# Optimization experiments

Hardware: AMD Instinct MI355X
Metric: run time of the kernel (lower is better)

The kernel has to match this reference:

```python
import jax, jax.numpy as jnp
import numpy as np

B, T, DM, DK = 16, 2048, 1024, 128

def setup_inputs() -> dict:
    key = jax.random.key(0)
    k1, k2, k3, k4 = jax.random.split(key, 4)
    x = jax.random.normal(k1, (B, T, DM), dtype=jnp.float32)
    # Linear(dm, dk, bias=False) weights, stored as [dm, dk] for x @ W
    scale = 1.0 / np.sqrt(DM)
    W_q = jax.random.normal(k2, (DM, DK), dtype=jnp.float32) * scale
    W_k = jax.random.normal(k3, (DM, DK), dtype=jnp.float32) * scale
    W_v = jax.random.normal(k4, (DM, DK), dtype=jnp.float32) * scale
    return {"x": x, "W_q": W_q, "W_k": W_k, "W_v": W_v}

def reference(x, W_q, W_k, W_v):
    # q, k, v: [B, T, DK]
    q = jnp.einsum('btd,dk->btk', x, W_q)
    k = jnp.einsum('btd,dk->btk', x, W_k)
    v = jnp.einsum('btd,dk->btk', x, W_v)
    dk = k.shape[-1]
    # scores: [B, T, T], scaled by dk**-0.5
    wei = jnp.einsum('bqk,bsk->bqs', q, k) * (dk ** -0.5)
    # causal mask (tril == 0 -> -inf)
    causal = jnp.tril(jnp.ones((q.shape[1], q.shape[1]), dtype=bool))
    wei = jnp.where(causal, wei, -jnp.inf)
    wei = jax.nn.softmax(wei, axis=-1)
    out = jnp.einsum('bqs,bsk->bqk', wei, v)  # [B, T, DK]
    return out
```

## Files before the change

kernel.cpp:

```cpp
#include <hip/hip_runtime.h>
#include <hip/hip_bf16.h>

#define NB 16
#define NT 2048
#define NDM 1024
#define NDK 128

typedef __bf16 bf16;
typedef bf16 bf16x4 __attribute__((ext_vector_type(4)));
typedef bf16 bf16x8 __attribute__((ext_vector_type(8)));
typedef float f32x4 __attribute__((ext_vector_type(4)));

__device__ inline bf16 to_bf16(float f) {
    __hip_bfloat16 h = __float2bfloat16(f);
    return *reinterpret_cast<bf16*>(&h);
}

__device__ inline void gload_lds16(const void* g, void* l) {
    __builtin_amdgcn_global_load_lds(
        (const __attribute__((address_space(1))) unsigned int*)g,
        (__attribute__((address_space(3))) unsigned int*)l, 16, 0, 0);
}

#define VMCNT(n) asm volatile("s_waitcnt vmcnt(" #n ")" ::: "memory")
#define LGKM0()  asm volatile("s_waitcnt lgkmcnt(0)" ::: "memory")
#define SCHEDB() __builtin_amdgcn_sched_barrier(0)

__global__ __launch_bounds__(256) void transpose_w_kernel(
        const float* __restrict__ Wq, const float* __restrict__ Wk,
        const float* __restrict__ Wv, bf16* __restrict__ Wt) {
    int idx = blockIdx.x * 256 + threadIdx.x;
    int w = idx >> 17;
    int r = idx & (NDM * NDK - 1);
    int k = r >> 7;
    int n = r & (NDK - 1);
    const float* W = (w == 0) ? Wq : ((w == 1) ? Wk : Wv);
    Wt[(size_t)w * NDK * NDM + (size_t)n * NDM + k] = to_bf16(W[(size_t)k * NDK + n]);
}

__global__ __launch_bounds__(512, 2) void proj_fused_kernel(
        const float* __restrict__ x, const bf16* __restrict__ Wt,
        bf16* __restrict__ qkv, bf16* __restrict__ Vt) {
    __shared__ __align__(16) char smem[65536];
    const int tid = threadIdx.x;
    const int lane = tid & 63, wave = tid >> 6;
    const int wr = wave >> 2, wc = wave & 3;
    const int r16 = lane & 15, kg = lane >> 4;
    const int mb = blockIdx.x;
    const float* xA = x + (size_t)mb * 128 * NDM;

    auto ASB = [&](int b) -> bf16* { return (bf16*)(smem + b * 8192); };
    auto BSB = [&](int b) -> bf16* { return (bf16*)(smem + 16384 + b * 24576); };

    const int a_row = tid >> 2, a_c = tid & 3;
    const int a_dst = (a_row * 4 + (a_c ^ ((a_row >> 1) & 3))) * 8;
    const size_t a_src = (size_t)a_row * NDM + a_c * 8;

    float4 alo, ahi;
    auto loadA = [&](int kt) {
        const float* src = xA + a_src + kt * 32;
        alo = *reinterpret_cast<const float4*>(src);
        ahi = *reinterpret_cast<const float4*>(src + 4);
    };
    auto writeA = [&](int buf) {
        bf16x8 v;
        v[0] = to_bf16(alo.x); v[1] = to_bf16(alo.y); v[2] = to_bf16(alo.z); v[3] = to_bf16(alo.w);
        v[4] = to_bf16(ahi.x); v[5] = to_bf16(ahi.y); v[6] = to_bf16(ahi.z); v[7] = to_bf16(ahi.w);
        *reinterpret_cast<bf16x8*>(ASB(buf) + a_dst) = v;
    };
    auto stageB = [&](int buf, int kt) {
#pragma unroll
        for (int p = 0; p < 3; p++) {
            int cid = p * 512 + tid;
            int w = cid >> 9, rem = cid & 511;
            int row = rem >> 2, c = rem & 3;
            int cs = c ^ ((row >> 1) & 3);
            gload_lds16(Wt + (size_t)w * NDK * NDM + (size_t)row * NDM + kt * 32 + cs * 8,
                        BSB(buf) + (size_t)(p * 512 + wave * 64) * 8);
        }
    };

    f32x4 acc[3][4][2];
#pragma unroll
    for (int w = 0; w < 3; w++)
#pragma unroll
        for (int m = 0; m < 4; m++)
#pragma unroll
            for (int n = 0; n < 2; n++) acc[w][m][n] = (f32x4){0.f, 0.f, 0.f, 0.f};

    loadA(0); SCHEDB(); stageB(0, 0); SCHEDB();
    VMCNT(3);
    writeA(0);
    loadA(1); SCHEDB(); stageB(1, 1); SCHEDB();
    VMCNT(5);
    LGKM0();
    __builtin_amdgcn_s_barrier();

    for (int kt = 0; kt < 32; kt++) {
        const int cur = kt & 1;
        bf16x8 af[4];
#pragma unroll
        for (int m = 0; m < 4; m++) {
            int arow = wr * 64 + m * 16 + r16;
            int ch = kg ^ ((arow >> 1) & 3);
            af[m] = *reinterpret_cast<const bf16x8*>(ASB(cur) + (arow * 4 + ch) * 8);
        }
#pragma unroll
        for (int w = 0; w < 3; w++) {
#pragma unroll
            for (int n = 0; n < 2; n++) {
                int brow = wc * 32 + n * 16 + r16;
                int ch = kg ^ ((brow >> 1) & 3);
                bf16x8 bfw = *reinterpret_cast<const bf16x8*>(
                    BSB(cur) + ((w * 128 + brow) * 4 + ch) * 8);
#pragma unroll
                for (int m = 0; m < 4; m++)
                    acc[w][m][n] = __builtin_amdgcn_mfma_f32_16x16x32_bf16(af[m], bfw, acc[w][m][n], 0, 0, 0);
            }
        }

        if (kt + 1 < 32) {
            VMCNT(3);
            writeA(1 - cur);
            LGKM0();
            __builtin_amdgcn_s_barrier();
            if (kt + 2 < 32) {
                loadA(kt + 2); SCHEDB(); stageB(cur, kt + 2); SCHEDB();
                VMCNT(5);
            } else {
                VMCNT(0);
            }
        }
    }

    __syncthreads();
    bf16 (*Tl)[136] = reinterpret_cast<bf16(*)[136]>(smem);
#pragma unroll
    for (int w = 0; w < 2; w++) {
        bf16* outw = qkv + (size_t)w * (size_t)(NB * NT) * NDK;
#pragma unroll
        for (int m = 0; m < 4; m++) {
            int rowb = mb * 128 + wr * 64 + m * 16 + kg * 4;
#pragma unroll
            for (int n = 0; n < 2; n++) {
                int col = wc * 32 + n * 16 + r16;
#pragma unroll
                for (int r = 0; r < 4; r++)
                    outw[(size_t)(rowb + r) * NDK + col] = to_bf16(acc[w][m][n][r]);
            }
        }
    }
#pragma unroll
    for (int m = 0; m < 4; m++) {
        int tl = wr * 64 + m * 16 + kg * 4;
#pragma unroll
        for (int n = 0; n < 2; n++) {
            int d = wc * 32 + n * 16 + r16;
            bf16x4 pv = { to_bf16(acc[2][m][n][0]), to_bf16(acc[2][m][n][1]),
                          to_bf16(acc[2][m][n][2]), to_bf16(acc[2][m][n][3]) };
            *reinterpret_cast<bf16x4*>(&Tl[d][tl]) = pv;
        }
    }
    __syncthreads();
    const int b = mb >> 4;
    const int t0 = (mb & 15) * 128;
    bf16* Vb = Vt + (size_t)b * NDK * NT;
#pragma unroll
    for (int p = 0; p < 4; p++) {
        int idx = p * 512 + tid;
        int d = idx >> 4, c = idx & 15;
        *reinterpret_cast<bf16x8*>(&Vb[(size_t)d * NT + t0 + c * 8]) =
            *reinterpret_cast<const bf16x8*>(&Tl[d][c * 8]);
    }
}

__global__ __launch_bounds__(256) void attn_kernel(
        const bf16* __restrict__ Q, const bf16* __restrict__ K,
        const bf16* __restrict__ Vt, float* __restrict__ out) {
    __shared__ bf16 Ks[2][64][128];
    __shared__ bf16 Vs[2][128][64];
    __shared__ bf16 Ps[4][16][72];
    const int tid = threadIdx.x, lane = tid & 63, wave = tid >> 6;
    const int r16 = lane & 15, kg = lane >> 4;

    const int bid = blockIdx.x;
    const int xcd = bid & 7;
    const int j = bid >> 3;
    const int b = xcd * 2 + (j & 1);
    const int qb = (NT / 64 - 1) - (j >> 1);
    const int q0 = qb * 64;
    const size_t baseB = (size_t)b * NT * NDK;
    const size_t baseVt = (size_t)b * NDK * NT;

    const float scale = 0.08838834764831843f;
    bf16x8 qf[4];
    const int qglob = q0 + wave * 16 + r16;
#pragma unroll
    for (int kc = 0; kc < 4; kc++) {
        bf16x8 raw = *reinterpret_cast<const bf16x8*>(&Q[baseB + (size_t)qglob * NDK + kc * 32 + kg * 8]);
#pragma unroll
        for (int jj = 0; jj < 8; jj++) raw[jj] = to_bf16((float)raw[jj] * scale);
        qf[kc] = raw;
    }

    f32x4 o[8];
#pragma unroll
    for (int n = 0; n < 8; n++) o[n] = (f32x4){0.f, 0.f, 0.f, 0.f};
    float mrun = -INFINITY;
    float lrun = 0.f;

    int krow[4], kcol[4], vrow[4], vcol[4];
#pragma unroll
    for (int i = 0; i < 4; i++) {
        int idx = i * 256 + tid;
        krow[i] = idx >> 4; kcol[i] = idx & 15;
        vrow[i] = idx >> 3; vcol[i] = idx & 7;
    }

    const int nsteps = qb + 1;
    bf16x8 kreg[4], vreg[4];
#pragma unroll
    for (int i = 0; i < 4; i++) {
        kreg[i] = *reinterpret_cast<const bf16x8*>(&K[baseB + (size_t)krow[i] * NDK + kcol[i] * 8]);
        vreg[i] = *reinterpret_cast<const bf16x8*>(&Vt[baseVt + (size_t)vrow[i] * NT + vcol[i] * 8]);
    }
#pragma unroll
    for (int i = 0; i < 4; i++) {
        *reinterpret_cast<bf16x8*>(&Ks[0][krow[i]][(kcol[i] ^ (krow[i] & 7)) * 8]) = kreg[i];
        *reinterpret_cast<bf16x8*>(&Vs[0][vrow[i]][(vcol[i] ^ (vrow[i] & 7)) * 8]) = vreg[i];
    }
    if (nsteps > 1) {
#pragma unroll
        for (int i = 0; i < 4; i++) {
            kreg[i] = *reinterpret_cast<const bf16x8*>(&K[baseB + (size_t)(64 + krow[i]) * NDK + kcol[i] * 8]);
            vreg[i] = *reinterpret_cast<const bf16x8*>(&Vt[baseVt + (size_t)vrow[i] * NT + 64 + vcol[i] * 8]);
        }
    }
    __syncthreads();

    for (int s = 0; s < nsteps; s++) {
        const int cur = s & 1;
        const int kv0 = s * 64;

        f32x4 sfr[4];
#pragma unroll
        for (int n = 0; n < 4; n++) sfr[n] = (f32x4){0.f, 0.f, 0.f, 0.f};
#pragma unroll
        for (int n = 0; n < 4; n++) {
            const int krw = n * 16 + r16;
#pragma unroll
            for (int kc = 0; kc < 4; kc++) {
                bf16x8 kf = *reinterpret_cast<const bf16x8*>(&Ks[cur][krw][((kc * 4 + kg) ^ (krw & 7)) * 8]);
                sfr[n] = __builtin_amdgcn_mfma_f32_16x16x32_bf16(kf, qf[kc], sfr[n], 0, 0, 0);
            }
        }

        if (s == nsteps - 1) {
#pragma unroll
            for (int n = 0; n < 4; n++)
#pragma unroll
                for (int r = 0; r < 4; r++)
                    if (kv0 + n * 16 + kg * 4 + r > qglob) sfr[n][r] = -INFINITY;
        }

        float pm = -INFINITY;
#pragma unroll
        for (int n = 0; n < 4; n++) {
            float t0 = fmaxf(fmaxf(sfr[n][0], sfr[n][1]), fmaxf(sfr[n][2], sfr[n][3]));
            pm = fmaxf(pm, t0);
        }
        pm = fmaxf(pm, __shfl_xor(pm, 16, 64));
        pm = fmaxf(pm, __shfl_xor(pm, 32, 64));

        if (__any(pm > mrun)) {
            float mnew = fmaxf(mrun, pm);
            float corr = __expf(mrun - mnew);
            mrun = mnew;
            lrun *= corr;
            float co[4];
#pragma unroll
            for (int r = 0; r < 4; r++) co[r] = __shfl(corr, kg * 4 + r, 64);
#pragma unroll
            for (int n = 0; n < 8; n++)
#pragma unroll
                for (int r = 0; r < 4; r++) o[n][r] *= co[r];
        }

        float ps = 0.f;
#pragma unroll
        for (int n = 0; n < 4; n++) {
            bf16x4 pw;
#pragma unroll
            for (int r = 0; r < 4; r++) {
                float pv = __expf(sfr[n][r] - mrun);
                ps += pv;
                pw[r] = to_bf16(pv);
            }
            *reinterpret_cast<bf16x4*>(&Ps[wave][r16][n * 16 + kg * 4]) = pw;
        }
        ps += __shfl_xor(ps, 16, 64);
        ps += __shfl_xor(ps, 32, 64);
        lrun += ps;

#pragma unroll
        for (int kc2 = 0; kc2 < 2; kc2++) {
            bf16x8 pf = *reinterpret_cast<const bf16x8*>(&Ps[wave][r16][kc2 * 32 + kg * 8]);
#pragma unroll
            for (int n = 0; n < 8; n++) {
                const int vrw = n * 16 + r16;
                bf16x8 vf = *reinterpret_cast<const bf16x8*>(&Vs[cur][vrw][((kc2 * 4 + kg) ^ (vrw & 7)) * 8]);
                o[n] = __builtin_amdgcn_mfma_f32_16x16x32_bf16(pf, vf, o[n], 0, 0, 0);
            }
        }

        if (s + 1 < nsteps) {
#pragma unroll
            for (int i = 0; i < 4; i++) {
                *reinterpret_cast<bf16x8*>(&Ks[1 - cur][krow[i]][(kcol[i] ^ (krow[i] & 7)) * 8]) = kreg[i];
                *reinterpret_cast<bf16x8*>(&Vs[1 - cur][vrow[i]][(vcol[i] ^ (vrow[i] & 7)) * 8]) = vreg[i];
            }
            if (s + 2 < nsteps) {
                const int kv2 = (s + 2) * 64;
#pragma unroll
                for (int i = 0; i < 4; i++) {
                    kreg[i] = *reinterpret_cast<const bf16x8*>(&K[baseB + (size_t)(kv2 + krow[i]) * NDK + kcol[i] * 8]);
                    vreg[i] = *reinterpret_cast<const bf16x8*>(&Vt[baseVt + (size_t)vrow[i] * NT + kv2 + vcol[i] * 8]);
                }
            }
        }
        __syncthreads();
    }

    float linv = 1.0f / lrun;
    float li[4];
#pragma unroll
    for (int r = 0; r < 4; r++) li[r] = __shfl(linv, kg * 4 + r, 64);
#pragma unroll
    for (int n = 0; n < 8; n++)
#pragma unroll
        for (int r = 0; r < 4; r++) {
            int row = q0 + wave * 16 + kg * 4 + r;
            int col = n * 16 + r16;
            out[baseB + (size_t)row * NDK + col] = o[n][r] * li[r];
        }
}

extern "C" void kernel_launch(void* const* d_in, const int* in_sizes, int n_in,
                              void* d_out, int out_size, void* d_ws, size_t ws_size,
                              hipStream_t stream) {
    const float* x  = (const float*)d_in[0];
    const float* Wq = (const float*)d_in[1];
    const float* Wk = (const float*)d_in[2];
    const float* Wv = (const float*)d_in[3];
    float* out = (float*)d_out;

    char* ws = (char*)d_ws;
    bf16* Wt  = (bf16*)ws;
    bf16* qkv = (bf16*)(ws + (1ull << 20));
    bf16* Vtg = (bf16*)(ws + (26ull << 20));

    transpose_w_kernel<<<(3 * NDM * NDK) / 256, 256, 0, stream>>>(Wq, Wk, Wv, Wt);

    proj_fused_kernel<<<(NB * NT) / 128, 512, 0, stream>>>(x, Wt, qkv, Vtg);

    bf16* Qp = qkv;
    bf16* Kp = qkv + (size_t)(NB * NT) * NDK;

    attn_kernel<<<dim3((NT / 64) * NB), 256, 0, stream>>>(Qp, Kp, Vtg, out);
}
```

Baseline: 101.5 us.

## Load x fragments directly into registers instead of staging through LDS

The projection kernel now has each wave load its own A (x) rows from global memory straight into MFMA operand registers and convert them to bf16 there, dropping the LDS staging buffer for A and its LDS writes and reads. The pipeline's vmcnt accounting and barrier placement are reworked, and B staging is now issued after the barrier. LDS use falls to 48KB and the two-blocks-per-CU launch bound is removed. In exchange, each x element is loaded from global memory by all four column waves rather than once per block, and register pressure rises from the eight float4 prefetch registers.

```diff
diff --git a/kernel.cpp b/kernel.cpp
--- a/kernel.cpp
+++ b/kernel.cpp
@@ -23,7 +23,6 @@
 }
 
 #define VMCNT(n) asm volatile("s_waitcnt vmcnt(" #n ")" ::: "memory")
-#define LGKM0()  asm volatile("s_waitcnt lgkmcnt(0)" ::: "memory")
 #define SCHEDB() __builtin_amdgcn_sched_barrier(0)
 
 __global__ __launch_bounds__(256) void transpose_w_kernel(
@@ -38,10 +37,10 @@
     Wt[(size_t)w * NDK * NDM + (size_t)n * NDM + k] = to_bf16(W[(size_t)k * NDK + n]);
 }
 
-__global__ __launch_bounds__(512, 2) void proj_fused_kernel(
+__global__ __launch_bounds__(512) void proj_fused_kernel(
         const float* __restrict__ x, const bf16* __restrict__ Wt,
         bf16* __restrict__ qkv, bf16* __restrict__ Vt) {
-    __shared__ __align__(16) char smem[65536];
+    __shared__ __align__(16) char smem[49152];
     const int tid = threadIdx.x;
     const int lane = tid & 63, wave = tid >> 6;
     const int wr = wave >> 2, wc = wave & 3;
@@ -49,25 +48,8 @@
     const int mb = blockIdx.x;
     const float* xA = x + (size_t)mb * 128 * NDM;
 
-    auto ASB = [&](int b) -> bf16* { return (bf16*)(smem + b * 8192); };
-    auto BSB = [&](int b) -> bf16* { return (bf16*)(smem + 16384 + b * 24576); };
-
-    const int a_row = tid >> 2, a_c = tid & 3;
-    const int a_dst = (a_row * 4 + (a_c ^ ((a_row >> 1) & 3))) * 8;
-    const size_t a_src = (size_t)a_row * NDM + a_c * 8;
-
-    float4 alo, ahi;
-    auto loadA = [&](int kt) {
-        const float* src = xA + a_src + kt * 32;
-        alo = *reinterpret_cast<const float4*>(src);
-        ahi = *reinterpret_cast<const float4*>(src + 4);
-    };
-    auto writeA = [&](int buf) {
-        bf16x8 v;
-        v[0] = to_bf16(alo.x); v[1] = to_bf16(alo.y); v[2] = to_bf16(alo.z); v[3] = to_bf16(alo.w);
-        v[4] = to_bf16(ahi.x); v[5] = to_bf16(ahi.y); v[6] = to_bf16(ahi.z); v[7] = to_bf16(ahi.w);
-        *reinterpret_cast<bf16x8*>(ASB(buf) + a_dst) = v;
-    };
+    auto BSB = [&](int b) -> bf16* { return (bf16*)(smem + b * 24576); };
+
     auto stageB = [&](int buf, int kt) {
 #pragma unroll
         for (int p = 0; p < 3; p++) {
@@ -80,6 +62,27 @@
         }
     };
 
+    float4 araw[8];
+    bf16x8 ac[4];
+    auto loadA = [&](int kt) {
+#pragma unroll
+        for (int m = 0; m < 4; m++) {
+            const float* p = xA + (size_t)(wr * 64 + m * 16 + r16) * NDM + kt * 32 + kg * 8;
+            araw[2 * m]     = *reinterpret_cast<const float4*>(p);
+            araw[2 * m + 1] = *reinterpret_cast<const float4*>(p + 4);
+        }
+    };
+    auto cvtA = [&]() {
+#pragma unroll
+        for (int m = 0; m < 4; m++) {
+            const float4 lo = araw[2 * m], hi = araw[2 * m + 1];
+            bf16x8 v;
+            v[0] = to_bf16(lo.x); v[1] = to_bf16(lo.y); v[2] = to_bf16(lo.z); v[3] = to_bf16(lo.w);
+            v[4] = to_bf16(hi.x); v[5] = to_bf16(hi.y); v[6] = to_bf16(hi.z); v[7] = to_bf16(hi.w);
+            ac[m] = v;
+        }
+    };
+
     f32x4 acc[3][4][2];
 #pragma unroll
     for (int w = 0; w < 3; w++)
@@ -88,23 +91,17 @@
 #pragma unroll
             for (int n = 0; n < 2; n++) acc[w][m][n] = (f32x4){0.f, 0.f, 0.f, 0.f};
 
-    loadA(0); SCHEDB(); stageB(0, 0); SCHEDB();
+    loadA(0); SCHEDB();
+    stageB(0, 0); SCHEDB();
     VMCNT(3);
-    writeA(0);
-    loadA(1); SCHEDB(); stageB(1, 1); SCHEDB();
-    VMCNT(5);
-    LGKM0();
+    cvtA();
+    loadA(1); SCHEDB();
+    stageB(1, 1); SCHEDB();
+    VMCNT(11);
     __builtin_amdgcn_s_barrier();
 
     for (int kt = 0; kt < 32; kt++) {
         const int cur = kt & 1;
-        bf16x8 af[4];
-#pragma unroll
-        for (int m = 0; m < 4; m++) {
-            int arow = wr * 64 + m * 16 + r16;
-            int ch = kg ^ ((arow >> 1) & 3);
-            af[m] = *reinterpret_cast<const bf16x8*>(ASB(cur) + (arow * 4 + ch) * 8);
-        }
 #pragma unroll
         for (int w = 0; w < 3; w++) {
 #pragma unroll
@@ -115,21 +112,21 @@
                     BSB(cur) + ((w * 128 + brow) * 4 + ch) * 8);
 #pragma unroll
                 for (int m = 0; m < 4; m++)
-                    acc[w][m][n] = __builtin_amdgcn_mfma_f32_16x16x32_bf16(af[m], bfw, acc[w][m][n], 0, 0, 0);
+                    acc[w][m][n] = __builtin_amdgcn_mfma_f32_16x16x32_bf16(ac[m], bfw, acc[w][m][n], 0, 0, 0);
             }
         }
 
         if (kt + 1 < 32) {
             VMCNT(3);
-            writeA(1 - cur);
-            LGKM0();
-            __builtin_amdgcn_s_barrier();
+            cvtA();
             if (kt + 2 < 32) {
-                loadA(kt + 2); SCHEDB(); stageB(cur, kt + 2); SCHEDB();
-                VMCNT(5);
+                loadA(kt + 2); SCHEDB();
+                VMCNT(8);
             } else {
                 VMCNT(0);
             }
+            __builtin_amdgcn_s_barrier();
+            if (kt + 2 < 32) { stageB(cur, kt + 2); SCHEDB(); }
         }
     }
 
```

Result: slower. 135.7 us (+33.8%).
